# Optimization experiments

Hardware: AMD Instinct MI355X
Metric: run time of the kernel (lower is better)

The kernel has to match this reference:

```python
import jax, jax.numpy as jnp
import numpy as np

B, DIM1, DIM2, DIM3 = 4, 2048, 4096, 4096


def setup_inputs() -> dict:
    key = jax.random.key(0)
    k1, k2, k3 = jax.random.split(key, 3)
    x = jax.random.normal(k1, (B, DIM1, DIM2), dtype=jnp.float32)
    y = jax.random.normal(k2, (B, DIM1, DIM3), dtype=jnp.float32)
    weight = jax.random.normal(k3, (DIM2, DIM3), dtype=jnp.float32)
    return {"x": x, "y": y, "weight": weight}


def reference(x, y, weight):
    # Out = hardswish(mish(leaky_relu(x @ W, 0.01) + y)) + 0.5
    v = jnp.einsum('bik,kn->bin', x, weight)              # (B, dim1, dim3)
    v = jnp.where(v >= 0, v, 0.01 * v)                    # LeakyReLU(0.01)
    v = v + y
    v = v * jnp.tanh(jax.nn.softplus(v))                  # Mish
    relu6 = jnp.clip(v + 3.0, 0.0, 6.0)
    v = v * relu6 * (1.0 / 6.0) + 0.5                     # HardSwish + 0.5 (baked into kernel)
    return v
```

## Files before the change

### kernel.cpp

```cpp
#include <hip/hip_runtime.h>
#include <hip/hip_bf16.h>
#include <cstdint>

typedef __attribute__((ext_vector_type(8))) short short8;
typedef __attribute__((ext_vector_type(4))) float f32x4;
typedef unsigned short ushort_t;

#define MM 8192
#define NN 4096
#define KK 4096

#define BM 128
#define BN 128
#define BK 64

#define MFMA_BF16 __builtin_amdgcn_mfma_f32_16x16x32_bf16

__device__ __forceinline__ ushort_t f2bf(float f) {
  uint32_t u = __builtin_bit_cast(uint32_t, f);
  u = (u + 0x7FFFu + ((u >> 16) & 1u)) >> 16;
  return (ushort_t)u;
}

__device__ __forceinline__ float epilogue(float v, float yv) {
  v = fmaxf(v, 0.01f * v);
  v += yv;
  const float vc = fminf(v, 15.f);
  const float t = __builtin_amdgcn_exp2f(vc * 1.44269504f);
  const float d = t * t + 2.f * t;
  const float mi = v * d * __builtin_amdgcn_rcpf(d + 2.f);
  const float r6 = fminf(fmaxf(mi + 3.f, 0.f), 6.f);
  return mi * r6 * (1.f / 6.f) + 0.5f;
}

__device__ __forceinline__ void gload_lds16(const void* g, void* l) {
  __builtin_amdgcn_global_load_lds(
      (const __attribute__((address_space(1))) unsigned int*)g,
      (__attribute__((address_space(3))) unsigned int*)l, 16, 0, 0);
}

#define CVT_BLOCKS ((MM * KK) / (256 * 8))
#define WT_BLOCKS ((NN / 32) * (KK / 32))

template <int DO_X>
__global__ void prep_kernel(const float* __restrict__ X, ushort_t* __restrict__ XB,
                            const float* __restrict__ W, ushort_t* __restrict__ WT) {
  __shared__ float t[32][33];
  const int bid = blockIdx.x;
  const int tid = threadIdx.x;
  if (DO_X && bid < CVT_BLOCKS) {
    const size_t i = ((size_t)bid * 256 + tid) * 8;
    f32x4 v0 = __builtin_nontemporal_load(reinterpret_cast<const f32x4*>(&X[i]));
    f32x4 v1 = __builtin_nontemporal_load(reinterpret_cast<const f32x4*>(&X[i + 4]));
    short8 o;
    o[0] = (short)f2bf(v0[0]); o[1] = (short)f2bf(v0[1]);
    o[2] = (short)f2bf(v0[2]); o[3] = (short)f2bf(v0[3]);
    o[4] = (short)f2bf(v1[0]); o[5] = (short)f2bf(v1[1]);
    o[6] = (short)f2bf(v1[2]); o[7] = (short)f2bf(v1[3]);
    *reinterpret_cast<short8*>(&XB[i]) = o;
  } else {
    const int b2 = DO_X ? (bid - CVT_BLOCKS) : bid;
    const int n0 = (b2 & 127) * 32, k0 = (b2 >> 7) * 32;
    const int tx = tid & 31, ty = tid >> 5;
#pragma unroll
    for (int i = ty; i < 32; i += 8)
      t[i][tx] = __builtin_nontemporal_load(&W[(size_t)(k0 + i) * NN + n0 + tx]);
    __syncthreads();
#pragma unroll
    for (int i = ty; i < 32; i += 8)
      WT[(size_t)(n0 + i) * KK + k0 + tx] = f2bf(t[tx][i]);
  }
}

__global__ __launch_bounds__(256, 4) void gemm_bf16(
    const ushort_t* __restrict__ XB, const ushort_t* __restrict__ WT,
    const float* __restrict__ Y, float* __restrict__ O) {
  __shared__ ushort_t As[BM * BK];
  __shared__ ushort_t Bs[BN * BK];

  const int wg = blockIdx.x;
  const int xcd = wg & 7;
  const int local = wg >> 3;
  const int bm0 = (local >> 2) * BM;
  const int bn0 = (xcd * 4 + (local & 3)) * BN;

  const int tid = threadIdx.x;
  const int lane = tid & 63;
  const int wid = tid >> 6;
  const int wm = (wid >> 1) * 64, wn = (wid & 1) * 64;
  const int lr = lane & 15, lg = lane >> 4, lr7 = lane & 7;

  const int s_sub = lane >> 3;
  const int s_chunk = (lane & 7) ^ s_sub;
  const int srow = wid * 32 + s_sub;
  const ushort_t* aB = XB + (size_t)(bm0 + srow) * KK + s_chunk * 8;
  const ushort_t* bB = WT + (size_t)(bn0 + srow) * KK + s_chunk * 8;
  ushort_t* aL = As + wid * 4 * 512;
  ushort_t* bL = Bs + wid * 4 * 512;

  const int aRow = (wm + lr) * BK;
  const int bRow = (wn + lr) * BK;
  const int slot0 = ((lg ^ lr7) << 3);
  const int slot1 = (((4 | lg) ^ lr7) << 3);
  const ushort_t* a0 = As + aRow + slot0;
  const ushort_t* a1 = As + aRow + slot1;
  const ushort_t* b0 = Bs + bRow + slot0;
  const ushort_t* b1 = Bs + bRow + slot1;

  f32x4 acc[4][4] = {};

  for (int kt = 0; kt < KK; kt += BK) {
    __syncthreads();
#pragma unroll
    for (int j = 0; j < 4; ++j)
      gload_lds16(aB + (size_t)j * 8 * KK + kt, aL + j * 512);
#pragma unroll
    for (int j = 0; j < 4; ++j)
      gload_lds16(bB + (size_t)j * 8 * KK + kt, bL + j * 512);
    __syncthreads();

#pragma unroll
    for (int ks = 0; ks < 2; ++ks) {
      const ushort_t* ap = ks ? a1 : a0;
      const ushort_t* bp = ks ? b1 : b0;
      short8 a[4], b[4];
#pragma unroll
      for (int i = 0; i < 4; ++i) {
        a[i] = *reinterpret_cast<const short8*>(ap + i * 16 * BK);
        b[i] = *reinterpret_cast<const short8*>(bp + i * 16 * BK);
      }
#pragma unroll
      for (int i = 0; i < 4; ++i)
#pragma unroll
        for (int j = 0; j < 4; ++j)
          acc[i][j] = MFMA_BF16(a[i], b[j], acc[i][j], 0, 0, 0);
    }
  }

#pragma unroll
  for (int i = 0; i < 4; ++i) {
#pragma unroll
    for (int j = 0; j < 4; ++j) {
#pragma unroll
      for (int r = 0; r < 4; ++r) {
        const int grow = bm0 + wm + i * 16 + lg * 4 + r;
        const int gcol = bn0 + wn + j * 16 + lr;
        const size_t idx = (size_t)grow * NN + gcol;
        const float yv = __builtin_nontemporal_load(&Y[idx]);
        __builtin_nontemporal_store(epilogue(acc[i][j][r], yv), &O[idx]);
      }
    }
  }
}

#define LDP 72
__global__ __launch_bounds__(256, 3) void gemm_fused(
    const float* __restrict__ X, const ushort_t* __restrict__ WT,
    const float* __restrict__ Y, float* __restrict__ O) {
  __shared__ ushort_t Asm[BM * LDP];
  __shared__ ushort_t Bsm[BN * LDP];

  const int nwg = (MM / BM) * (NN / BN);
  int wg = blockIdx.x;
  wg = (wg % 8) * (nwg / 8) + wg / 8;
  const int NT = NN / BN;
  const int bm0 = (wg / NT) * BM;
  const int bn0 = (wg % NT) * BN;

  const int tid = threadIdx.x;
  const int lane = tid & 63;
  const int wid = tid >> 6;
  const int wm = (wid >> 1) * 64, wn = (wid & 1) * 64;
  const int lr = lane & 15, lg = lane >> 4;

  f32x4 acc[4][4] = {};

  const int arow = tid >> 2;
  const int ac = (tid & 3) * 4;
  const int brow = tid >> 1;
  const int bc0 = (tid & 1) * 32;

  for (int kt = 0; kt < KK; kt += BK) {
    __syncthreads();
#pragma unroll
    for (int p = 0; p < 2; ++p) {
      const int row = arow + p * 64;
      const float* src = &X[(size_t)(bm0 + row) * KK + kt];
#pragma unroll
      for (int j = 0; j < 4; ++j) {
        f32x4 v = *reinterpret_cast<const f32x4*>(&src[ac + j * 16]);
        uint2 packed;
        packed.x = (uint32_t)f2bf(v[0]) | ((uint32_t)f2bf(v[1]) << 16);
        packed.y = (uint32_t)f2bf(v[2]) | ((uint32_t)f2bf(v[3]) << 16);
        *reinterpret_cast<uint2*>(&Asm[row * LDP + ac + j * 16]) = packed;
      }
    }
    {
      const ushort_t* src = &WT[(size_t)(bn0 + brow) * KK + kt + bc0];
#pragma unroll
      for (int j = 0; j < 4; ++j) {
        short8 u = *reinterpret_cast<const short8*>(&src[j * 8]);
        *reinterpret_cast<short8*>(&Bsm[brow * LDP + bc0 + j * 8]) = u;
      }
    }
    __syncthreads();

#pragma unroll
    for (int ks = 0; ks < 2; ++ks) {
      short8 a[4], b[4];
#pragma unroll
      for (int i = 0; i < 4; ++i) {
        a[i] = *reinterpret_cast<const short8*>(&Asm[(wm + i * 16 + lr) * LDP + ks * 32 + lg * 8]);
        b[i] = *reinterpret_cast<const short8*>(&Bsm[(wn + i * 16 + lr) * LDP + ks * 32 + lg * 8]);
      }
#pragma unroll
      for (int i = 0; i < 4; ++i)
#pragma unroll
        for (int j = 0; j < 4; ++j)
          acc[i][j] = MFMA_BF16(a[i], b[j], acc[i][j], 0, 0, 0);
    }
  }

#pragma unroll
  for (int i = 0; i < 4; ++i) {
#pragma unroll
    for (int j = 0; j < 4; ++j) {
#pragma unroll
      for (int r = 0; r < 4; ++r) {
        const int grow = bm0 + wm + i * 16 + lg * 4 + r;
        const int gcol = bn0 + wn + j * 16 + lr;
        const size_t idx = (size_t)grow * NN + gcol;
        O[idx] = epilogue(acc[i][j][r], Y[idx]);
      }
    }
  }
}

__global__ void naive_fused(const float* __restrict__ X, const float* __restrict__ W,
                            const float* __restrict__ Y, float* __restrict__ O) {
  const int n0 = (blockIdx.x * 256 + threadIdx.x) * 4;
  const int m = blockIdx.y;
  f32x4 acc = {0.f, 0.f, 0.f, 0.f};
  const float* xr = &X[(size_t)m * KK];
  for (int k = 0; k < KK; ++k) {
    const float xv = xr[k];
    const f32x4 wv = *reinterpret_cast<const f32x4*>(&W[(size_t)k * NN + n0]);
    acc[0] += xv * wv[0];
    acc[1] += xv * wv[1];
    acc[2] += xv * wv[2];
    acc[3] += xv * wv[3];
  }
  const size_t idx = (size_t)m * NN + n0;
  O[idx + 0] = epilogue(acc[0], Y[idx + 0]);
  O[idx + 1] = epilogue(acc[1], Y[idx + 1]);
  O[idx + 2] = epilogue(acc[2], Y[idx + 2]);
  O[idx + 3] = epilogue(acc[3], Y[idx + 3]);
}

extern "C" void kernel_launch(void* const* d_in, const int* in_sizes, int n_in,
                              void* d_out, int out_size, void* d_ws, size_t ws_size,
                              hipStream_t stream) {
  const float* x = (const float*)d_in[0];
  const float* y = (const float*)d_in[1];
  const float* w = (const float*)d_in[2];
  float* out = (float*)d_out;

  const size_t xb_bytes = (size_t)MM * KK * sizeof(ushort_t);
  const size_t wt_bytes = (size_t)NN * KK * sizeof(ushort_t);

  if (ws_size >= xb_bytes + wt_bytes) {
    ushort_t* XB = (ushort_t*)d_ws;
    ushort_t* WT = (ushort_t*)((char*)d_ws + xb_bytes);
    hipLaunchKernelGGL((prep_kernel<1>), dim3(CVT_BLOCKS + WT_BLOCKS), dim3(256), 0, stream,
                       x, XB, w, WT);
    hipLaunchKernelGGL(gemm_bf16, dim3((MM / BM) * (NN / BN)), dim3(256), 0, stream,
                       XB, WT, y, out);
  } else if (ws_size >= wt_bytes) {
    ushort_t* WT = (ushort_t*)d_ws;
    hipLaunchKernelGGL((prep_kernel<0>), dim3(WT_BLOCKS), dim3(256), 0, stream,
                       x, nullptr, w, WT);
    hipLaunchKernelGGL(gemm_fused, dim3((MM / BM) * (NN / BN)), dim3(256), 0, stream,
                       x, WT, y, out);
  } else {
    hipLaunchKernelGGL(naive_fused, dim3(NN / 1024, MM), dim3(256), 0, stream, x, w, y, out);
  }
}
```

Measured before the change: 339.6 us.

## Double-buffer LDS tiles in bf16 GEMM to overlap global loads with MFMA

```diff
diff --git a/kernel.cpp b/kernel.cpp
--- a/kernel.cpp
+++ b/kernel.cpp
@@ -13,6 +13,7 @@
 #define BM 128
 #define BN 128
 #define BK 64
+#define NT (KK / BK)
 
 #define MFMA_BF16 __builtin_amdgcn_mfma_f32_16x16x32_bf16
 
@@ -72,11 +73,11 @@
   }
 }
 
-__global__ __launch_bounds__(256, 4) void gemm_bf16(
+__global__ __launch_bounds__(256, 2) void gemm_bf16_d(
     const ushort_t* __restrict__ XB, const ushort_t* __restrict__ WT,
     const float* __restrict__ Y, float* __restrict__ O) {
-  __shared__ ushort_t As[BM * BK];
-  __shared__ ushort_t Bs[BN * BK];
+  __shared__ ushort_t As[2 * BM * BK];
+  __shared__ ushort_t Bs[2 * BN * BK];
 
   const int wg = blockIdx.x;
   const int xcd = wg & 7;
@@ -92,11 +93,13 @@
 
   const int s_sub = lane >> 3;
   const int s_chunk = (lane & 7) ^ s_sub;
-  const int srow = wid * 32 + s_sub;
-  const ushort_t* aB = XB + (size_t)(bm0 + srow) * KK + s_chunk * 8;
-  const ushort_t* bB = WT + (size_t)(bn0 + srow) * KK + s_chunk * 8;
-  ushort_t* aL = As + wid * 4 * 512;
-  ushort_t* bL = Bs + wid * 4 * 512;
+  uint32_t offA[4], offB[4];
+#pragma unroll
+  for (int j = 0; j < 4; ++j) {
+    const int srow = wid * 32 + j * 8 + s_sub;
+    offA[j] = (uint32_t)(bm0 + srow) * KK + s_chunk * 8;
+    offB[j] = (uint32_t)(bn0 + srow) * KK + s_chunk * 8;
+  }
 
   const int aRow = (wm + lr) * BK;
   const int bRow = (wn + lr) * BK;
@@ -109,33 +112,46 @@
 
   f32x4 acc[4][4] = {};
 
-  for (int kt = 0; kt < KK; kt += BK) {
-    __syncthreads();
-#pragma unroll
-    for (int j = 0; j < 4; ++j)
-      gload_lds16(aB + (size_t)j * 8 * KK + kt, aL + j * 512);
-#pragma unroll
-    for (int j = 0; j < 4; ++j)
-      gload_lds16(bB + (size_t)j * 8 * KK + kt, bL + j * 512);
-    __syncthreads();
-
-#pragma unroll
-    for (int ks = 0; ks < 2; ++ks) {
-      const ushort_t* ap = ks ? a1 : a0;
-      const ushort_t* bp = ks ? b1 : b0;
-      short8 a[4], b[4];
-#pragma unroll
-      for (int i = 0; i < 4; ++i) {
-        a[i] = *reinterpret_cast<const short8*>(ap + i * 16 * BK);
-        b[i] = *reinterpret_cast<const short8*>(bp + i * 16 * BK);
-      }
-#pragma unroll
-      for (int i = 0; i < 4; ++i)
-#pragma unroll
-        for (int j = 0; j < 4; ++j)
-          acc[i][j] = MFMA_BF16(a[i], b[j], acc[i][j], 0, 0, 0);
-    }
-  }
+#define STAGE(buf, kv)                                                         \
+  _Pragma("unroll") for (int j = 0; j < 4; ++j) {                              \
+    gload_lds16(XB + offA[j] + (kv), As + (buf) * 8192 + (wid * 4 + j) * 512); \
+    gload_lds16(WT + offB[j] + (kv), Bs + (buf) * 8192 + (wid * 4 + j) * 512); \
+  }
+
+#define COMPUTE(buf)                                                           \
+  _Pragma("unroll") for (int ks = 0; ks < 2; ++ks) {                           \
+    const ushort_t* ap = ks ? a1 : a0;                                         \
+    const ushort_t* bp = ks ? b1 : b0;                                         \
+    short8 a[4], b[4];                                                         \
+    _Pragma("unroll") for (int i = 0; i < 4; ++i) {                            \
+      a[i] = *reinterpret_cast<const short8*>(ap + (buf) * 8192 + i * 1024);   \
+      b[i] = *reinterpret_cast<const short8*>(bp + (buf) * 8192 + i * 1024);   \
+    }                                                                          \
+    _Pragma("unroll") for (int i = 0; i < 4; ++i)                              \
+        _Pragma("unroll") for (int j = 0; j < 4; ++j)                          \
+            acc[i][j] = MFMA_BF16(a[i], b[j], acc[i][j], 0, 0, 0);             \
+  }
+
+#define KSTEP(cur, nxt, t)                                                     \
+  {                                                                            \
+    const int k1 = (((t) + 1) & (NT - 1)) * BK;                                \
+    STAGE(nxt, k1);                     \
+    COMPUTE(cur);                                                              \
+    __syncthreads();    \
+  }
+
+  STAGE(0, 0);
+  __syncthreads();
+
+#pragma unroll 1
+  for (int t = 0; t < NT; t += 2) {
+    KSTEP(0, 1, t);
+    KSTEP(1, 0, t + 1);
+  }
+
+#undef STAGE
+#undef COMPUTE
+#undef KSTEP
 
 #pragma unroll
   for (int i = 0; i < 4; ++i) {
@@ -163,9 +179,9 @@
   const int nwg = (MM / BM) * (NN / BN);
   int wg = blockIdx.x;
   wg = (wg % 8) * (nwg / 8) + wg / 8;
-  const int NT = NN / BN;
-  const int bm0 = (wg / NT) * BM;
-  const int bn0 = (wg % NT) * BN;
+  const int NTC = NN / BN;
+  const int bm0 = (wg / NTC) * BM;
+  const int bn0 = (wg % NTC) * BN;
 
   const int tid = threadIdx.x;
   const int lane = tid & 63;
@@ -273,7 +289,7 @@
     ushort_t* WT = (ushort_t*)((char*)d_ws + xb_bytes);
     hipLaunchKernelGGL((prep_kernel<1>), dim3(CVT_BLOCKS + WT_BLOCKS), dim3(256), 0, stream,
                        x, XB, w, WT);
-    hipLaunchKernelGGL(gemm_bf16, dim3((MM / BM) * (NN / BN)), dim3(256), 0, stream,
+    hipLaunchKernelGGL(gemm_bf16_d, dim3((MM / BM) * (NN / BN)), dim3(256), 0, stream,
                        XB, WT, y, out);
   } else if (ws_size >= wt_bytes) {
     ushort_t* WT = (ushort_t*)d_ws;
```

After: 410.2 us. +20.8%, slower.
